# Optimization experiments

Measured on AMD Instinct MI355X. Metric: run time of the kernel, lower is better.

Reference implementation:

```python
import jax, jax.numpy as jnp
import numpy as np

N_NODES = 20000
NEG_SLOPE = 0.2
EPS = 1e-10


def _gat_reparam_layer(x, W, att_i, att_j, bias, src, dst, heads, c2):
    """GATConv (PyG-style, aggr='add') whose output encodes (mean, std) per head,
    followed by diag-Gaussian reparameterization with N(0,1) prior (eval mode:
    output = mean; ixz = KL(q||p) summed over channels, averaged over heads).
    x: [N, F]; W: [F, heads*c2]; att_i/att_j: [heads, c2]; bias: [heads*c2].
    c2 = 2 * out_channels (mean + std logits).
    Returns out [N, heads*(c2//2)], ixz [N]."""
    N = x.shape[0]
    h = (x @ W).reshape(N, heads, c2)                      # [N, H, 2C]
    h_i = h[dst]                                           # [E, H, 2C] target (x_i)
    h_j = h[src]                                           # [E, H, 2C] source (x_j)
    # attention logits: leaky_relu((x_i*att_i).sum + (x_j*att_j).sum)
    logits = jnp.sum(h_i * att_i, axis=-1) + jnp.sum(h_j * att_j, axis=-1)  # [E, H]
    logits = jax.nn.leaky_relu(logits, NEG_SLOPE)
    # segment softmax over incoming edges of each target node
    lmax = jax.ops.segment_max(logits, dst, num_segments=N)  # [N, H]
    ex = jnp.exp(logits - lmax[dst])                         # [E, H]
    denom = jax.ops.segment_sum(ex, dst, num_segments=N)     # [N, H]
    alpha = ex / denom[dst]                                  # [E, H]
    # weighted scatter-add aggregation
    msg = alpha[:, :, None] * h_j                            # [E, H, 2C]
    out = jax.ops.segment_sum(msg, dst, num_segments=N)      # [N, H, 2C]
    out = out + bias.reshape(1, heads, c2)
    # reparameterization: split per head into mean / std
    C = c2 // 2
    mean = out[..., :C]                                      # [N, H, C]
    std = jax.nn.softplus(out[..., C:]) + EPS                # [N, H, C]
    # KL(N(mean, std) || N(0, 1)) per element, sum over C, mean over heads
    kl = 0.5 * (std * std + mean * mean - 1.0) - jnp.log(std)
    ixz = kl.sum(-1).mean(-1)                                # [N]
    return mean.reshape(N, heads * C), ixz


def setup_inputs() -> dict:
    key = jax.random.key(0)
    ks = jax.random.split(key, 10)
    N, F1 = N_NODES, 256
    E = 320000
    H1, C1 = 8, 32    # conv1: latent_size//2 = 32 per head, doubled for (mean,std)
    H2, C2 = 1, 16    # conv2: num_classes = 16
    edge_index = jax.random.randint(ks[0], (2, E), 0, N, dtype=jnp.int32)
    s = 0.1
    return {
        "x": jax.random.normal(ks[1], (N, F1), jnp.float32),
        "edge_index": edge_index,
        "W1": jax.random.normal(ks[2], (F1, H1 * 2 * C1), jnp.float32) * s,
        "att_i1": jax.random.normal(ks[3], (H1, 2 * C1), jnp.float32) * s,
        "att_j1": jax.random.normal(ks[4], (H1, 2 * C1), jnp.float32) * s,
        "bias1": jax.random.normal(ks[5], (H1 * 2 * C1,), jnp.float32) * s,
        "W2": jax.random.normal(ks[6], (H1 * C1, H2 * 2 * C2), jnp.float32) * s,
        "att_i2": jax.random.normal(ks[7], (H2, 2 * C2), jnp.float32) * s,
        "att_j2": jax.random.normal(ks[8], (H2, 2 * C2), jnp.float32) * s,
        "bias2": jax.random.normal(ks[9], (H2 * 2 * C2,), jnp.float32) * s,
    }


def reference(x, edge_index, W1, att_i1, att_j1, bias1, W2, att_i2, att_j2, bias2):
    src, dst = edge_index[0], edge_index[1]
    # eval mode: dropout is identity, output = posterior mean (val_use_mean=True)
    h1, ixz1 = _gat_reparam_layer(x, W1, att_i1, att_j1, bias1, src, dst, heads=8, c2=64)
    h1 = jax.nn.elu(h1)
    h2, ixz2 = _gat_reparam_layer(h1, W2, att_i2, att_j2, bias2, src, dst, heads=1, c2=32)
    return h2
```

## Files before the change

kernel.cpp:

```cpp
#include <hip/hip_runtime.h>
#include <hip/hip_bf16.h>

#define NN 20000
#define EE 320000
#define NEG_SLOPE 0.2f
#define CAP1 96
#define BCAP 128

typedef unsigned short u16;
typedef short bf16x8 __attribute__((ext_vector_type(8)));
typedef unsigned short u16x8 __attribute__((ext_vector_type(8)));
typedef float f32x4 __attribute__((ext_vector_type(4)));

__device__ __forceinline__ u16 f2bf(float f) {
    unsigned u = __float_as_uint(f);
    return (u16)((u + 0x7FFFu + ((u >> 16) & 1u)) >> 16);
}
__device__ __forceinline__ float bf2f(u16 b) { return __uint_as_float(((unsigned)b) << 16); }

__device__ __forceinline__ void lds_fence() {
    asm volatile("s_waitcnt lgkmcnt(0)" ::: "memory");
}

#define IB_W1 320
#define IB_W2 338
#define IB_CU 417
#define IB_XB 2917
__global__ __launch_bounds__(256) void init_pack(
    const float* __restrict__ x,
    const float* __restrict__ W1, const float* __restrict__ atti1, const float* __restrict__ attj1,
    const float* __restrict__ W2, const float* __restrict__ atti2, const float* __restrict__ attj2,
    u16* __restrict__ Wp1, u16* __restrict__ Wp2, int* __restrict__ cursor, u16* __restrict__ xb)
{
    int b = blockIdx.x;
    if (b < IB_W1) {
        int t = b*256 + threadIdx.x;
        int k = t & 255, j = t >> 8;
        float v = 0.f;
        if (j < 256) {
            v = W1[(size_t)k*512 + ((j>>5)*64 + (j&31))];
        } else if (j < 264) {
            int h = j - 256; float s = 0.f;
            for (int c = 0; c < 64; ++c) s += W1[(size_t)k*512 + h*64 + c] * atti1[h*64 + c];
            v = s;
        } else if (j < 272) {
            int h = j - 264; float s = 0.f;
            for (int c = 0; c < 64; ++c) s += W1[(size_t)k*512 + h*64 + c] * attj1[h*64 + c];
            v = s;
        }
        Wp1[t] = f2bf(v);
    } else if (b < IB_W2) {
        int j = b - IB_W1;
        int k = threadIdx.x;
        float v;
        if (j < 16) {
            v = W2[(size_t)k*32 + j];
        } else if (j == 16) {
            float s = 0.f; for (int c = 0; c < 32; ++c) s += W2[(size_t)k*32 + c] * atti2[c]; v = s;
        } else {
            float s = 0.f; for (int c = 0; c < 32; ++c) s += W2[(size_t)k*32 + c] * attj2[c]; v = s;
        }
        Wp2[j*256 + k] = f2bf(v);
    } else if (b < IB_CU) {
        int i = (b - IB_W2)*256 + threadIdx.x;
        if (i < NN) cursor[i] = 0;
    } else {
        size_t gb = ((size_t)(b - IB_CU)*256 + threadIdx.x) * 8;
        float4 v0 = *(const float4*)&x[gb];
        float4 v1 = *(const float4*)&x[gb + 4];
        u16x8 u;
        u[0]=f2bf(v0.x); u[1]=f2bf(v0.y); u[2]=f2bf(v0.z); u[3]=f2bf(v0.w);
        u[4]=f2bf(v1.x); u[5]=f2bf(v1.y); u[6]=f2bf(v1.z); u[7]=f2bf(v1.w);
        *(u16x8*)&xb[gb] = u;
    }
}

__device__ __forceinline__ void gemm_body(
    int bx, int by, int tid,
    const u16* __restrict__ Ab, const u16* __restrict__ Bp, int M,
    u16* __restrict__ outB, float* __restrict__ outAi, float* __restrict__ outAj)
{
    __shared__ __align__(16) u16 lsA[64*64];
    __shared__ __align__(16) u16 lsB[64*64];

    const int w    = tid >> 6, lane = tid & 63;
    const int brow = by * 64, bcol = bx * 64;

    const int srow = tid >> 2;
    const int kseg = (tid & 3) * 16;
    const int aRow = min(brow + srow, M-1);
    const int s0   = kseg >> 3;
    const int wOff0 = srow*64 + ((s0    ) ^ (srow & 7))*8;
    const int wOff1 = srow*64 + ((s0 + 1) ^ (srow & 7))*8;

    const int frow = (w << 4) + (lane & 15);
    const int fkb  = lane >> 4;
    int aF[2], bF[2][4];
    #pragma unroll
    for (int v = 0; v < 2; ++v) {
        aF[v] = frow*64 + (((v*4 + fkb) ^ (frow & 7)))*8;
        #pragma unroll
        for (int tt = 0; tt < 4; ++tt) {
            int col = tt*16 + (lane & 15);
            bF[v][tt] = col*64 + (((v*4 + fkb) ^ (col & 7)))*8;
        }
    }

    f32x4 acc[4] = {};

    for (int ks = 0; ks < 4; ++ks) {
        const int k0 = ks*64;
        const u16* ap = Ab + (size_t)aRow*256 + k0 + kseg;
        *(u16x8*)&lsA[wOff0] = *(const u16x8*)(ap);
        *(u16x8*)&lsA[wOff1] = *(const u16x8*)(ap+8);
        const u16* bp = Bp + (size_t)(bcol + srow)*256 + k0 + kseg;
        *(u16x8*)&lsB[wOff0] = *(const u16x8*)(bp);
        *(u16x8*)&lsB[wOff1] = *(const u16x8*)(bp+8);
        __syncthreads();
        #pragma unroll
        for (int v = 0; v < 2; ++v) {
            bf16x8 a = *(const bf16x8*)&lsA[aF[v]];
            #pragma unroll
            for (int tt = 0; tt < 4; ++tt) {
                bf16x8 b = *(const bf16x8*)&lsB[bF[v][tt]];
                acc[tt] = __builtin_amdgcn_mfma_f32_16x16x32_bf16(a, b, acc[tt], 0, 0, 0);
            }
        }
        __syncthreads();
    }

    #pragma unroll
    for (int tt = 0; tt < 4; ++tt) {
        int col = bcol + tt*16 + (lane & 15);
        #pragma unroll
        for (int r = 0; r < 4; ++r) {
            int row = brow + (w << 4) + ((lane >> 4) << 2) + r;
            if (row >= M) continue;
            float v = acc[tt][r];
            if      (col < 256) outB[(size_t)row*256 + col] = f2bf(v);
            else if (col < 264) outAi[(size_t)row*8 + (col - 256)] = v;
            else if (col < 272) outAj[(size_t)row*8 + (col - 264)] = v;
        }
    }
}

#define G1_BLOCKS 1565
#define SC_BLOCKS 1250

__global__ __launch_bounds__(256) void fusedA(
    const u16* __restrict__ xb, const u16* __restrict__ Wp1,
    u16* __restrict__ h1m, float* __restrict__ ai1, float* __restrict__ aj1,
    const int* __restrict__ src, const int* __restrict__ dst,
    int* __restrict__ cursor, int* __restrict__ elist)
{
    int b = blockIdx.x;
    if (b < G1_BLOCKS) {
        gemm_body(b % 5, b / 5, threadIdx.x, xb, Wp1, NN, h1m, ai1, aj1);
    } else {
        int e = (b - G1_BLOCKS)*256 + threadIdx.x;
        if (e < EE) {
            int d = dst[e];
            int pos = atomicAdd(&cursor[d], 1);
            if (pos < BCAP) elist[d*BCAP + pos] = src[e];
        }
    }
}

__global__ __launch_bounds__(256) void gat1g2(
    const int* __restrict__ cursor, const int* __restrict__ elist,
    const float* __restrict__ ai, const float* __restrict__ aj,
    const u16* __restrict__ h1m, const float* __restrict__ bias,
    const u16* __restrict__ Wp2,
    float* __restrict__ h2m, float* __restrict__ ai2, float* __restrict__ aj2)
{
    __shared__ float s_w[4][CAP1*9];
    __shared__ int   s_src[4][CAP1];
    __shared__ float s_inv[4][8];

    const int wv = threadIdx.x >> 6, lane = threadIdx.x & 63;
    const int n = blockIdx.x*4 + wv;
    const int beg = n*BCAP;
    const int deg = min(cursor[n], BCAP);
    float* sw = s_w[wv];
    int*   ss = s_src[wv];

    float4 ai0 = *(const float4*)&ai[(size_t)n*8];
    float4 ai1v = *(const float4*)&ai[(size_t)n*8 + 4];
    float aiv[8] = {ai0.x,ai0.y,ai0.z,ai0.w,ai1v.x,ai1v.y,ai1v.z,ai1v.w};

    const int g = lane & 31, head = g >> 2, cbase = (g & 3)*8;
    float v[8];

    if (deg <= CAP1) {
        for (int e = lane; e < deg; e += 64) {
            int s = elist[beg + e];
            ss[e] = s;
            float4 a0 = *(const float4*)&aj[(size_t)s*8];
            float4 a1 = *(const float4*)&aj[(size_t)s*8 + 4];
            float av[8] = {a0.x,a0.y,a0.z,a0.w,a1.x,a1.y,a1.z,a1.w};
            #pragma unroll
            for (int h = 0; h < 8; ++h) {
                float l = aiv[h] + av[h];
                sw[e*9 + h] = (l >= 0.f) ? l : NEG_SLOPE * l;
            }
        }
        lds_fence();
        {
            int h = lane >> 3, sl = lane & 7;
            float mx = -INFINITY;
            for (int e = sl; e < deg; e += 8) mx = fmaxf(mx, sw[e*9 + h]);
            #pragma unroll
            for (int o = 1; o < 8; o <<= 1) mx = fmaxf(mx, __shfl_xor(mx, o, 64));
            float sm = 0.f;
            for (int e = sl; e < deg; e += 8) {
                float ex = __expf(sw[e*9 + h] - mx);
                sw[e*9 + h] = ex;
                sm += ex;
            }
            #pragma unroll
            for (int o = 1; o < 8; o <<= 1) sm += __shfl_xor(sm, o, 64);
            if (sl == 0) s_inv[wv][h] = (deg > 0) ? 1.f / sm : 0.f;
        }
        lds_fence();
        {
            int slot = lane >> 5;
            float inv = s_inv[wv][head];
            const u16* hb = h1m + (size_t)g*8;
            float acc[8] = {};
            int e = slot;
            for (; e + 6 < deg; e += 8) {
                int   i0 = ss[e],          i1 = ss[e+2],          i2 = ss[e+4],          i3 = ss[e+6];
                float w0 = sw[e*9+head],   w1 = sw[(e+2)*9+head], w2 = sw[(e+4)*9+head], w3 = sw[(e+6)*9+head];
                bf16x8 v0 = *(const bf16x8*)&hb[(size_t)i0*256];
                bf16x8 v1 = *(const bf16x8*)&hb[(size_t)i1*256];
                bf16x8 v2 = *(const bf16x8*)&hb[(size_t)i2*256];
                bf16x8 v3 = *(const bf16x8*)&hb[(size_t)i3*256];
                #pragma unroll
                for (int k = 0; k < 8; ++k) {
                    acc[k] += w0 * bf2f((u16)v0[k]);
                    acc[k] += w1 * bf2f((u16)v1[k]);
                    acc[k] += w2 * bf2f((u16)v2[k]);
                    acc[k] += w3 * bf2f((u16)v3[k]);
                }
            }
            for (; e < deg; e += 2) {
                float wgt = sw[e*9 + head];
                bf16x8 vx = *(const bf16x8*)&hb[(size_t)ss[e]*256];
                #pragma unroll
                for (int k = 0; k < 8; ++k)
                    acc[k] += wgt * bf2f((u16)vx[k]);
            }
            #pragma unroll
            for (int k = 0; k < 8; ++k) acc[k] += __shfl_xor(acc[k], 32, 64);
            #pragma unroll
            for (int k = 0; k < 8; ++k) {
                float t = acc[k]*inv + bias[head*64 + cbase + k];
                v[k] = (t > 0.f) ? t : (__expf(t) - 1.0f);
            }
        }
    } else {
        float* sh = sw;
        for (int h = 0; h < 8; ++h) {
            float a_i = aiv[h];
            float mx = -INFINITY;
            for (int e = lane; e < deg; e += 64) {
                int s = elist[beg + e];
                float t = a_i + aj[(size_t)s*8 + h];
                t = (t >= 0.f) ? t : NEG_SLOPE * t;
                mx = fmaxf(mx, t);
            }
            #pragma unroll
            for (int o = 32; o > 0; o >>= 1) mx = fmaxf(mx, __shfl_xor(mx, o, 64));
            float sm = 0.f;
            for (int e = lane; e < deg; e += 64) {
                int s = elist[beg + e];
                float t = a_i + aj[(size_t)s*8 + h];
                t = (t >= 0.f) ? t : NEG_SLOPE * t;
                sm += __expf(t - mx);
            }
            #pragma unroll
            for (int o = 32; o > 0; o >>= 1) sm += __shfl_xor(sm, o, 64);
            float inv = (deg > 0) ? 1.f / sm : 0.f;
            int c = lane & 31, sl2 = lane >> 5;
            float a2 = 0.f;
            for (int e = sl2; e < deg; e += 2) {
                int s = elist[beg + e];
                float t = a_i + aj[(size_t)s*8 + h];
                t = (t >= 0.f) ? t : NEG_SLOPE * t;
                float wgt = __expf(t - mx);
                a2 += wgt * bf2f(h1m[(size_t)s*256 + h*32 + c]);
            }
            a2 += __shfl_xor(a2, 32, 64);
            if (lane < 32) {
                float t = a2*inv + bias[h*64 + c];
                sh[h*32 + c] = (t > 0.f) ? t : (__expf(t) - 1.0f);
            }
        }
        lds_fence();
        #pragma unroll
        for (int k = 0; k < 8; ++k) v[k] = sh[g*8 + k];
    }

    {
        int jbase = (lane >> 5) * 9;
        float p[9];
        #pragma unroll
        for (int jj = 0; jj < 9; ++jj) {
            u16x8 wr = *(const u16x8*)&Wp2[(size_t)(jbase + jj)*256 + g*8];
            float s = 0.f;
            #pragma unroll
            for (int k = 0; k < 8; ++k) s += v[k] * bf2f((u16)wr[k]);
            p[jj] = s;
        }
        #pragma unroll
        for (int o = 1; o < 32; o <<= 1) {
            #pragma unroll
            for (int jj = 0; jj < 9; ++jj) p[jj] += __shfl_xor(p[jj], o, 64);
        }
        float outv = p[0];
        #pragma unroll
        for (int jj = 1; jj < 9; ++jj) if (g == jj) outv = p[jj];
        if (g < 9) {
            int j = jbase + g;
            if      (j < 16)  h2m[(size_t)n*16 + j] = outv;
            else if (j == 16) ai2[n] = outv;
            else if (j == 17) aj2[n] = outv;
        }
    }
}

__global__ __launch_bounds__(256) void gat2_fused(
    const int* __restrict__ cursor, const int* __restrict__ elist,
    const float* __restrict__ ai, const float* __restrict__ aj,
    const float* __restrict__ h2m, const float* __restrict__ bias,
    float* __restrict__ outp)
{
    __shared__ float s_w2[4][64];
    __shared__ int   s_s2[4][64];

    const int wv = threadIdx.x >> 6, lane = threadIdx.x & 63;
    const int n = blockIdx.x*4 + wv;
    const int beg = n*BCAP;
    const int deg = min(cursor[n], BCAP);
    float a_i = ai[n];

    if (deg <= 64) {
        float l = -INFINITY; int s = 0;
        if (lane < deg) {
            s = elist[beg + lane];
            float t = a_i + aj[s];
            l = (t >= 0.f) ? t : NEG_SLOPE * t;
        }
        float mx = l;
        #pragma unroll
        for (int o = 32; o > 0; o >>= 1) mx = fmaxf(mx, __shfl_xor(mx, o, 64));
        float ex = (lane < deg) ? __expf(l - mx) : 0.f;
        float sm = ex;
        #pragma unroll
        for (int o = 32; o > 0; o >>= 1) sm += __shfl_xor(sm, o, 64);
        float inv = (deg > 0) ? 1.f / sm : 0.f;
        if (lane < deg) { s_w2[wv][lane] = ex; s_s2[wv][lane] = s; }
        lds_fence();
        int c4 = lane & 3, slot = lane >> 2;
        float4 acc = make_float4(0.f, 0.f, 0.f, 0.f);
        for (int e = slot; e < deg; e += 16) {
            float w = s_w2[wv][e];
            int sv = s_s2[wv][e];
            float4 vv = *(const float4*)&h2m[(size_t)sv*16 + c4*4];
            acc.x += w*vv.x; acc.y += w*vv.y; acc.z += w*vv.z; acc.w += w*vv.w;
        }
        #pragma unroll
        for (int o = 4; o <= 32; o <<= 1) {
            acc.x += __shfl_xor(acc.x, o, 64);
            acc.y += __shfl_xor(acc.y, o, 64);
            acc.z += __shfl_xor(acc.z, o, 64);
            acc.w += __shfl_xor(acc.w, o, 64);
        }
        if (lane < 4) {
            const float4 b4 = *(const float4*)&bias[lane*4];
            float4 r = make_float4(acc.x*inv + b4.x, acc.y*inv + b4.y,
                                   acc.z*inv + b4.z, acc.w*inv + b4.w);
            *(float4*)&outp[(size_t)n*16 + lane*4] = r;
        }
    } else {
        float mx = -INFINITY;
        for (int e = lane; e < deg; e += 64) {
            int s2 = elist[beg + e];
            float t = a_i + aj[s2];
            t = (t >= 0.f) ? t : NEG_SLOPE * t;
            mx = fmaxf(mx, t);
        }
        #pragma unroll
        for (int o = 32; o > 0; o >>= 1) mx = fmaxf(mx, __shfl_xor(mx, o, 64));
        float sm = 0.f;
        for (int e = lane; e < deg; e += 64) {
            int s2 = elist[beg + e];
            float t = a_i + aj[s2];
            t = (t >= 0.f) ? t : NEG_SLOPE * t;
            sm += __expf(t - mx);
        }
        #pragma unroll
        for (int o = 32; o > 0; o >>= 1) sm += __shfl_xor(sm, o, 64);
        float inv = (deg > 0) ? 1.f / sm : 0.f;
        int c = lane & 15, e4 = lane >> 4;
        float acc = 0.f;
        for (int e = e4; e < deg; e += 4) {
            int s2 = elist[beg + e];
            float t = a_i + aj[s2];
            t = (t >= 0.f) ? t : NEG_SLOPE * t;
            float w = __expf(t - mx);
            acc += w * h2m[(size_t)s2*16 + c];
        }
        acc += __shfl_xor(acc, 16, 64);
        acc += __shfl_xor(acc, 32, 64);
        if (lane < 16) outp[(size_t)n*16 + lane] = acc*inv + bias[lane];
    }
}

static inline size_t al16(size_t x) { return (x + 15) & ~(size_t)15; }

extern "C" void kernel_launch(void* const* d_in, const int* in_sizes, int n_in,
                              void* d_out, int out_size, void* d_ws, size_t ws_size,
                              hipStream_t stream) {
    const float* x      = (const float*)d_in[0];
    const int*   ei     = (const int*)  d_in[1];
    const float* W1     = (const float*)d_in[2];
    const float* att_i1 = (const float*)d_in[3];
    const float* att_j1 = (const float*)d_in[4];
    const float* bias1  = (const float*)d_in[5];
    const float* W2     = (const float*)d_in[6];
    const float* att_i2 = (const float*)d_in[7];
    const float* att_j2 = (const float*)d_in[8];
    const float* bias2  = (const float*)d_in[9];
    float* out = (float*)d_out;

    const int N = NN, E = EE;
    const int* src = ei;
    const int* dst = ei + E;

    char* p = (char*)d_ws;
    #define CARVE(ty, name, elems) ty* name = (ty*)p; p += al16((size_t)(elems) * sizeof(ty));
    CARVE(u16,   Wp1,  320*256)
    CARVE(u16,   Wp2,  18*256)
    CARVE(u16,   xb,   (size_t)N*256)
    CARVE(u16,   h1m,  (size_t)N*256)
    CARVE(float, ai1,  (size_t)N*8)
    CARVE(float, aj1,  (size_t)N*8)
    CARVE(float, h2m,  (size_t)N*16)
    CARVE(float, ai2,  N)
    CARVE(float, aj2,  N)
    CARVE(int,   cursor,   N)
    CARVE(int,   elist,    (size_t)N*BCAP)
    #undef CARVE

    const int BS = 256;

    init_pack<<<IB_XB, BS, 0, stream>>>(x, W1, att_i1, att_j1, W2, att_i2, att_j2,
                                        Wp1, Wp2, cursor, xb);

    fusedA<<<G1_BLOCKS + SC_BLOCKS, BS, 0, stream>>>(xb, Wp1, h1m, ai1, aj1,
                                                     src, dst, cursor, elist);

    gat1g2<<<N/4, BS, 0, stream>>>(cursor, elist, ai1, aj1, h1m, bias1, Wp2,
                                   h2m, ai2, aj2);

    gat2_fused<<<N/4, BS, 0, stream>>>(cursor, elist, ai2, aj2, h2m, bias2, out);
}
```

Measured before the change: 79.93 us.

## Fuse x bf16 conversion into GEMM load and deepen gather unrolling

The separate pass that converts x to bf16 in init_pack is removed. The GEMM now reads fp32 x directly and converts it while staging tiles into LDS, which drops one full write and read of the bf16 copy. In gat1g2, the per-edge logit computation is spread so four lanes each handle two heads of one edge, and the aggregation loop gains an 8-edge unrolled stage to keep more gathers in flight. The cost is that each GEMM block reads twice as many bytes for A, since x is read 5 times across the column blocks, and the unrolled loop uses more registers.

Result: slower. 85.49 us (+7.0%).

```diff
diff --git a/kernel.cpp b/kernel.cpp
--- a/kernel.cpp
+++ b/kernel.cpp
@@ -25,12 +25,10 @@
 #define IB_W1 320
 #define IB_W2 338
 #define IB_CU 417
-#define IB_XB 2917
 __global__ __launch_bounds__(256) void init_pack(
-    const float* __restrict__ x,
     const float* __restrict__ W1, const float* __restrict__ atti1, const float* __restrict__ attj1,
     const float* __restrict__ W2, const float* __restrict__ atti2, const float* __restrict__ attj2,
-    u16* __restrict__ Wp1, u16* __restrict__ Wp2, int* __restrict__ cursor, u16* __restrict__ xb)
+    u16* __restrict__ Wp1, u16* __restrict__ Wp2, int* __restrict__ cursor)
 {
     int b = blockIdx.x;
     if (b < IB_W1) {
@@ -61,23 +59,15 @@
             float s = 0.f; for (int c = 0; c < 32; ++c) s += W2[(size_t)k*32 + c] * attj2[c]; v = s;
         }
         Wp2[j*256 + k] = f2bf(v);
-    } else if (b < IB_CU) {
+    } else {
         int i = (b - IB_W2)*256 + threadIdx.x;
         if (i < NN) cursor[i] = 0;
-    } else {
-        size_t gb = ((size_t)(b - IB_CU)*256 + threadIdx.x) * 8;
-        float4 v0 = *(const float4*)&x[gb];
-        float4 v1 = *(const float4*)&x[gb + 4];
-        u16x8 u;
-        u[0]=f2bf(v0.x); u[1]=f2bf(v0.y); u[2]=f2bf(v0.z); u[3]=f2bf(v0.w);
-        u[4]=f2bf(v1.x); u[5]=f2bf(v1.y); u[6]=f2bf(v1.z); u[7]=f2bf(v1.w);
-        *(u16x8*)&xb[gb] = u;
     }
 }
 
 __device__ __forceinline__ void gemm_body(
     int bx, int by, int tid,
-    const u16* __restrict__ Ab, const u16* __restrict__ Bp, int M,
+    const float* __restrict__ x, const u16* __restrict__ Bp, int M,
     u16* __restrict__ outB, float* __restrict__ outAi, float* __restrict__ outAj)
 {
     __shared__ __align__(16) u16 lsA[64*64];
@@ -110,9 +100,16 @@
 
     for (int ks = 0; ks < 4; ++ks) {
         const int k0 = ks*64;
-        const u16* ap = Ab + (size_t)aRow*256 + k0 + kseg;
-        *(u16x8*)&lsA[wOff0] = *(const u16x8*)(ap);
-        *(u16x8*)&lsA[wOff1] = *(const u16x8*)(ap+8);
+        const float* ap = x + (size_t)aRow*256 + k0 + kseg;
+        float4 v0 = *(const float4*)(ap+0),  v1 = *(const float4*)(ap+4);
+        float4 v2 = *(const float4*)(ap+8),  v3 = *(const float4*)(ap+12);
+        u16x8 u0, u1;
+        u0[0]=f2bf(v0.x); u0[1]=f2bf(v0.y); u0[2]=f2bf(v0.z); u0[3]=f2bf(v0.w);
+        u0[4]=f2bf(v1.x); u0[5]=f2bf(v1.y); u0[6]=f2bf(v1.z); u0[7]=f2bf(v1.w);
+        u1[0]=f2bf(v2.x); u1[1]=f2bf(v2.y); u1[2]=f2bf(v2.z); u1[3]=f2bf(v2.w);
+        u1[4]=f2bf(v3.x); u1[5]=f2bf(v3.y); u1[6]=f2bf(v3.z); u1[7]=f2bf(v3.w);
+        *(u16x8*)&lsA[wOff0] = u0;
+        *(u16x8*)&lsA[wOff1] = u1;
         const u16* bp = Bp + (size_t)(bcol + srow)*256 + k0 + kseg;
         *(u16x8*)&lsB[wOff0] = *(const u16x8*)(bp);
         *(u16x8*)&lsB[wOff1] = *(const u16x8*)(bp+8);
@@ -148,14 +145,14 @@
 #define SC_BLOCKS 1250
 
 __global__ __launch_bounds__(256) void fusedA(
-    const u16* __restrict__ xb, const u16* __restrict__ Wp1,
+    const float* __restrict__ x, const u16* __restrict__ Wp1,
     u16* __restrict__ h1m, float* __restrict__ ai1, float* __restrict__ aj1,
     const int* __restrict__ src, const int* __restrict__ dst,
     int* __restrict__ cursor, int* __restrict__ elist)
 {
     int b = blockIdx.x;
     if (b < G1_BLOCKS) {
-        gemm_body(b % 5, b / 5, threadIdx.x, xb, Wp1, NN, h1m, ai1, aj1);
+        gemm_body(b % 5, b / 5, threadIdx.x, x, Wp1, NN, h1m, ai1, aj1);
     } else {
         int e = (b - G1_BLOCKS)*256 + threadIdx.x;
         if (e < EE) {
@@ -184,24 +181,24 @@
     float* sw = s_w[wv];
     int*   ss = s_src[wv];
 
-    float4 ai0 = *(const float4*)&ai[(size_t)n*8];
-    float4 ai1v = *(const float4*)&ai[(size_t)n*8 + 4];
-    float aiv[8] = {ai0.x,ai0.y,ai0.z,ai0.w,ai1v.x,ai1v.y,ai1v.z,ai1v.w};
-
     const int g = lane & 31, head = g >> 2, cbase = (g & 3)*8;
     float v[8];
 
     if (deg <= CAP1) {
-        for (int e = lane; e < deg; e += 64) {
-            int s = elist[beg + e];
-            ss[e] = s;
-            float4 a0 = *(const float4*)&aj[(size_t)s*8];
-            float4 a1 = *(const float4*)&aj[(size_t)s*8 + 4];
-            float av[8] = {a0.x,a0.y,a0.z,a0.w,a1.x,a1.y,a1.z,a1.w};
-            #pragma unroll
-            for (int h = 0; h < 8; ++h) {
-                float l = aiv[h] + av[h];
-                sw[e*9 + h] = (l >= 0.f) ? l : NEG_SLOPE * l;
+        {
+            int hq = lane & 3, eo = lane >> 2;
+            float2 aip = *(const float2*)&ai[(size_t)n*8 + hq*2];
+            for (int e0 = 0; e0 < deg; e0 += 16) {
+                int e = e0 + eo;
+                if (e < deg) {
+                    int s = elist[beg + e];
+                    float2 a = *(const float2*)&aj[(size_t)s*8 + hq*2];
+                    float l0 = aip.x + a.x;
+                    float l1 = aip.y + a.y;
+                    sw[e*9 + 2*hq]     = (l0 >= 0.f) ? l0 : NEG_SLOPE * l0;
+                    sw[e*9 + 2*hq + 1] = (l1 >= 0.f) ? l1 : NEG_SLOPE * l1;
+                    if (hq == 0) ss[e] = s;
+                }
             }
         }
         lds_fence();
@@ -228,20 +225,29 @@
             const u16* hb = h1m + (size_t)g*8;
             float acc[8] = {};
             int e = slot;
+            for (; e + 14 < deg; e += 16) {
+                int ii[8]; float ww[8];
+                #pragma unroll
+                for (int j = 0; j < 8; ++j) { ii[j] = ss[e + 2*j]; ww[j] = sw[(e + 2*j)*9 + head]; }
+                bf16x8 vv[8];
+                #pragma unroll
+                for (int j = 0; j < 8; ++j) vv[j] = *(const bf16x8*)&hb[(size_t)ii[j]*256];
+                #pragma unroll
+                for (int j = 0; j < 8; ++j)
+                    #pragma unroll
+                    for (int k = 0; k < 8; ++k) acc[k] += ww[j] * bf2f((u16)vv[j][k]);
+            }
             for (; e + 6 < deg; e += 8) {
-                int   i0 = ss[e],          i1 = ss[e+2],          i2 = ss[e+4],          i3 = ss[e+6];
-                float w0 = sw[e*9+head],   w1 = sw[(e+2)*9+head], w2 = sw[(e+4)*9+head], w3 = sw[(e+6)*9+head];
-                bf16x8 v0 = *(const bf16x8*)&hb[(size_t)i0*256];
-                bf16x8 v1 = *(const bf16x8*)&hb[(size_t)i1*256];
-                bf16x8 v2 = *(const bf16x8*)&hb[(size_t)i2*256];
-                bf16x8 v3 = *(const bf16x8*)&hb[(size_t)i3*256];
-                #pragma unroll
-                for (int k = 0; k < 8; ++k) {
-                    acc[k] += w0 * bf2f((u16)v0[k]);
-                    acc[k] += w1 * bf2f((u16)v1[k]);
-                    acc[k] += w2 * bf2f((u16)v2[k]);
-                    acc[k] += w3 * bf2f((u16)v3[k]);
-                }
+                int ii[4]; float ww[4];
+                #pragma unroll
+                for (int j = 0; j < 4; ++j) { ii[j] = ss[e + 2*j]; ww[j] = sw[(e + 2*j)*9 + head]; }
+                bf16x8 vv[4];
+                #pragma unroll
+                for (int j = 0; j < 4; ++j) vv[j] = *(const bf16x8*)&hb[(size_t)ii[j]*256];
+                #pragma unroll
+                for (int j = 0; j < 4; ++j)
+                    #pragma unroll
+                    for (int k = 0; k < 8; ++k) acc[k] += ww[j] * bf2f((u16)vv[j][k]);
             }
             for (; e < deg; e += 2) {
                 float wgt = sw[e*9 + head];
@@ -260,6 +266,9 @@
         }
     } else {
         float* sh = sw;
+        float4 ai0 = *(const float4*)&ai[(size_t)n*8];
+        float4 ai1v = *(const float4*)&ai[(size_t)n*8 + 4];
+        float aiv[8] = {ai0.x,ai0.y,ai0.z,ai0.w,ai1v.x,ai1v.y,ai1v.z,ai1v.w};
         for (int h = 0; h < 8; ++h) {
             float a_i = aiv[h];
             float mx = -INFINITY;
@@ -442,7 +451,6 @@
     #define CARVE(ty, name, elems) ty* name = (ty*)p; p += al16((size_t)(elems) * sizeof(ty));
     CARVE(u16,   Wp1,  320*256)
     CARVE(u16,   Wp2,  18*256)
-    CARVE(u16,   xb,   (size_t)N*256)
     CARVE(u16,   h1m,  (size_t)N*256)
     CARVE(float, ai1,  (size_t)N*8)
     CARVE(float, aj1,  (size_t)N*8)
@@ -455,10 +463,10 @@
 
     const int BS = 256;
 
-    init_pack<<<IB_XB, BS, 0, stream>>>(x, W1, att_i1, att_j1, W2, att_i2, att_j2,
-                                        Wp1, Wp2, cursor, xb);
-
-    fusedA<<<G1_BLOCKS + SC_BLOCKS, BS, 0, stream>>>(xb, Wp1, h1m, ai1, aj1,
+    init_pack<<<IB_CU, BS, 0, stream>>>(W1, att_i1, att_j1, W2, att_i2, att_j2,
+                                        Wp1, Wp2, cursor);
+
+    fusedA<<<G1_BLOCKS + SC_BLOCKS, BS, 0, stream>>>(x, Wp1, h1m, ai1, aj1,
                                                      src, dst, cursor, elist);
 
     gat1g2<<<N/4, BS, 0, stream>>>(cursor, elist, ai1, aj1, h1m, bias1, Wp2,
```
